# Performance work log

Measured on AMD Instinct MI355X. Metric: run time of the kernel, lower is better.

The kernel has to match this reference:

```python
import jax, jax.numpy as jnp
import numpy as np

B, S, D_MODEL = 4, 2048, 1024
NUM_HEADS, HEAD_DIM = 16, 64
EPS = 1e-6


def setup_inputs() -> dict:
    key = jax.random.key(0)
    ks = jax.random.split(key, 6)
    hd = NUM_HEADS * HEAD_DIM
    scale_in = 1.0 / np.sqrt(D_MODEL)
    scale_hd = 1.0 / np.sqrt(hd)
    return {
        "x": jax.random.normal(ks[0], (B, S, D_MODEL), dtype=jnp.float32),
        "w_q": jax.random.normal(ks[1], (D_MODEL, hd), dtype=jnp.float32) * scale_in,
        "w_k": jax.random.normal(ks[2], (D_MODEL, hd), dtype=jnp.float32) * scale_in,
        "w_v": jax.random.normal(ks[3], (D_MODEL, hd), dtype=jnp.float32) * scale_in,
        "w_proj": jax.random.normal(ks[4], (hd, D_MODEL), dtype=jnp.float32) * scale_hd,
        "b_proj": jax.random.normal(ks[5], (D_MODEL,), dtype=jnp.float32) * 0.01,
        "ln_gamma": jnp.ones((D_MODEL,), dtype=jnp.float32),
        "ln_beta": jnp.zeros((D_MODEL,), dtype=jnp.float32),
    }


def reference(x, w_q, w_k, w_v, w_proj, b_proj, ln_gamma, ln_beta):
    # x: [B, S, D]; project and split heads -> [B, H, S, Dh]
    def split_heads(t):
        b, s, _ = t.shape
        return t.reshape(b, s, NUM_HEADS, HEAD_DIM).transpose(0, 2, 1, 3)

    q = split_heads(x @ w_q)
    k = split_heads(x @ w_k)
    v = split_heads(x @ w_v)

    scale = HEAD_DIM ** (-0.5)
    attn = jnp.einsum("bnqd,bnkd->bnqk", q, k) * scale  # [B, H, S, S]
    attn = jax.nn.softmax(attn, axis=-1)
    o = jnp.einsum("bnqk,bnkd->bnqd", attn, v)  # [B, H, S, Dh]
    o = o.transpose(0, 2, 1, 3).reshape(x.shape[0], x.shape[1], NUM_HEADS * HEAD_DIM)

    # proj + residual (dropout = identity in eval) then LayerNorm(eps=1e-6)
    y = o @ w_proj + b_proj + x
    mean = jnp.mean(y, axis=-1, keepdims=True)
    var = jnp.var(y, axis=-1, keepdims=True)
    y = (y - mean) * jax.lax.rsqrt(var + EPS) * ln_gamma + ln_beta
    return y
```

## Files before the change

kernel.cpp:

```cpp
#include <hip/hip_runtime.h>
#include <hip/hip_fp16.h>


typedef unsigned short u16;
typedef __attribute__((ext_vector_type(8))) u16 u16x8;
typedef __attribute__((ext_vector_type(4))) u16 u16x4;
typedef __attribute__((ext_vector_type(2))) unsigned int u32x2;
typedef __attribute__((ext_vector_type(8))) __bf16 bf16x8;
typedef __attribute__((ext_vector_type(8))) _Float16 f16x8;
typedef __attribute__((ext_vector_type(4))) _Float16 f16x4;
typedef __attribute__((ext_vector_type(2))) _Float16 f16x2;
typedef __attribute__((ext_vector_type(2))) __fp16 hf16x2;
typedef __attribute__((ext_vector_type(4))) float f32x4;

#define SM_C1 0.1803368801111204f

static __device__ __forceinline__ u16 f2bf(float f) {
  union { float f; unsigned int u; } v; v.f = f;
  unsigned int u = v.u;
  return (u16)((u + 0x7fffu + ((u >> 16) & 1u)) >> 16);
}
static __device__ __forceinline__ float bf2f(u16 b) {
  union { unsigned int u; float f; } v; v.u = ((unsigned int)b) << 16;
  return v.f;
}
static __device__ __forceinline__ u16 f2h(float f) {
  union { _Float16 h; u16 u; } v; v.h = (_Float16)f;
  return v.u;
}

static __device__ __forceinline__ void gld16(const u16* g, u16* l) {
  __builtin_amdgcn_global_load_lds((const __attribute__((address_space(1))) void*)g,
                                   (__attribute__((address_space(3))) void*)l, 16, 0, 0);
}

#define QBAR() do { asm volatile("" ::: "memory"); __builtin_amdgcn_s_barrier(); \
                    asm volatile("" ::: "memory"); } while (0)
#define QDRAIN() asm volatile("s_waitcnt vmcnt(0)" ::: "memory")
#define QWAIT6() asm volatile("s_waitcnt vmcnt(6)" ::: "memory")


__global__ __launch_bounds__(256) void k_convx(const float* __restrict__ x,
                                               u16* __restrict__ xbf) {
  int i = (blockIdx.x * 256 + threadIdx.x) * 8;
  float4 a = *(const float4*)(x + i);
  float4 b = *(const float4*)(x + i + 4);
  u16x8 o;
  o[0] = f2bf(a.x); o[1] = f2bf(a.y); o[2] = f2bf(a.z); o[3] = f2bf(a.w);
  o[4] = f2bf(b.x); o[5] = f2bf(b.y); o[6] = f2bf(b.z); o[7] = f2bf(b.w);
  *(u16x8*)(xbf + i) = o;
}

__global__ __launch_bounds__(256) void k_convwT(const float* __restrict__ w0,
                                                const float* __restrict__ w1,
                                                const float* __restrict__ w2,
                                                const float* __restrict__ w3,
                                                u16* __restrict__ o0, u16* __restrict__ o1,
                                                u16* __restrict__ o2, u16* __restrict__ o3) {
  __shared__ float tile[64][65];
  const float* w = blockIdx.z == 0 ? w0 : blockIdx.z == 1 ? w1 : blockIdx.z == 2 ? w2 : w3;
  u16* o = blockIdx.z == 0 ? o0 : blockIdx.z == 1 ? o1 : blockIdx.z == 2 ? o2 : o3;
  const int k0 = blockIdx.x * 64, n0 = blockIdx.y * 64;
  const int t = threadIdx.x;
#pragma unroll
  for (int i = 0; i < 16; i++) {
    int idx = t + 256 * i;
    int k = idx >> 6, n = idx & 63;
    tile[k][n] = w[(k0 + k) * 1024 + n0 + n];
  }
  __syncthreads();
#pragma unroll
  for (int i = 0; i < 16; i++) {
    int idx = t + 256 * i;
    int n = idx >> 6, k = idx & 63;
    o[(n0 + n) * 1024 + k0 + k] = f2bf(tile[k][n]);
  }
}


__global__ __launch_bounds__(512, 2) void k_gemm_qkv(const u16* __restrict__ xbf,
                                                     const u16* __restrict__ wT,
                                                     u16* __restrict__ Qb, u16* __restrict__ Kb,
                                                     u16* __restrict__ VbT) {
  __shared__ alignas(16) u16 As[2][256 * 64];
  __shared__ alignas(16) u16 Bs[2][128 * 64];
  const int t = threadIdx.x;
  const int wv = t >> 6, lane = t & 63, quad = lane >> 4, l16 = lane & 15;
  const int wm = wv >> 1, wn = wv & 1;
  const int m0 = blockIdx.x * 256;
  const int nt = blockIdx.y;
  const int srow = t >> 3;
  const int kg = (t & 7) ^ (srow & 7);
  const u16* aG = xbf + (size_t)(m0 + srow) * 1024 + kg * 8;
  const u16* bG = wT + (size_t)(nt * 128 + srow) * 1024 + kg * 8;
  const int sw = l16 & 7;
  const int ldsDst = wv * 512;

  f32x4 acc[4][4] = {};

  auto STAGE = [&](int tl) {
    const int p_ = tl & 1;
    const int k0_ = tl * 64;
#pragma unroll
    for (int i = 0; i < 4; i++)
      gld16(aG + (size_t)i * 64 * 1024 + k0_, &As[p_][i * 4096 + ldsDst]);
#pragma unroll
    for (int i = 0; i < 2; i++)
      gld16(bG + (size_t)i * 64 * 1024 + k0_, &Bs[p_][i * 4096 + ldsDst]);
  };

  STAGE(0);

#pragma unroll 2
  for (int tile = 0; tile < 16; ++tile) {
    const int p = tile & 1;
    if (tile < 15) { STAGE(tile + 1); QWAIT6(); }
    else           { QDRAIN(); }
    QBAR();

    bf16x8 a[4][2], b[4][2];
#pragma unroll
    for (int f = 0; f < 4; f++)
#pragma unroll
      for (int kk = 0; kk < 2; kk++)
        a[f][kk] = *(const bf16x8*)&As[p][(wm * 64 + f * 16 + l16) * 64 +
                                          ((kk * 4 + quad) ^ sw) * 8];
#pragma unroll
    for (int g = 0; g < 4; g++)
#pragma unroll
      for (int kk = 0; kk < 2; kk++)
        b[g][kk] = *(const bf16x8*)&Bs[p][(wn * 64 + g * 16 + l16) * 64 +
                                          ((kk * 4 + quad) ^ sw) * 8];
#pragma unroll
    for (int f = 0; f < 4; f++)
#pragma unroll
      for (int g = 0; g < 4; g++)
#pragma unroll
        for (int kk = 0; kk < 2; kk++)
          acc[f][g] = __builtin_amdgcn_mfma_f32_16x16x32_bf16(a[f][kk], b[g][kk], acc[f][g], 0, 0, 0);

    QBAR();
  }

  const int sel = nt >> 3;
  const int n0 = (nt & 7) * 128 + wn * 64;
  const int mBase = m0 + wm * 64 + quad * 4;
  if (sel < 2) {
    u16* Ob = sel == 0 ? Qb : Kb;
    const float scl = sel == 0 ? SM_C1 : 1.0f;
#pragma unroll
    for (int f = 0; f < 4; f++)
#pragma unroll
      for (int g = 0; g < 4; g++)
#pragma unroll
        for (int r = 0; r < 4; r++) {
          int m = mBase + f * 16 + r;
          int n = n0 + g * 16 + l16;
          Ob[(size_t)m * 1024 + n] = f2bf(acc[f][g][r] * scl);
        }
  } else {
#pragma unroll
    for (int f = 0; f < 4; f++) {
      int m = mBase + f * 16;
      int bb = m >> 11, s = m & 2047;
#pragma unroll
      for (int g = 0; g < 4; g++) {
        int n = n0 + g * 16 + l16;
        int hh = n >> 6, dh = n & 63;
        u16x4 o;
#pragma unroll
        for (int r = 0; r < 4; r++) o[r] = f2h(acc[f][g][r]);
        *(u16x4*)&VbT[(size_t)(((bb << 4) + hh) * 64 + dh) * 2048 + s] = o;
      }
    }
  }
}


__global__ __launch_bounds__(256) void k_gemm_proj(const u16* __restrict__ Abf,
                                                   const u16* __restrict__ wT,
                                                   const float* __restrict__ x,
                                                   const float* __restrict__ bias,
                                                   u16* __restrict__ ypre) {
  __shared__ alignas(16) u16 Als[128 * 64];
  __shared__ alignas(16) u16 Bls[128 * 64];
  const int t = threadIdx.x;
  const int wv = t >> 6, lane = t & 63, quad = lane >> 4, l16 = lane & 15;
  const int wm = wv >> 1, wn = wv & 1;
  const int m0 = blockIdx.x * 128;
  const int n0t = blockIdx.y * 128;
  const int row = t >> 3;
  const int kg = (t & 7) ^ (row & 7);
  const u16* aG = Abf + (size_t)(m0 + row) * 1024 + kg * 8;
  const u16* bG = wT + (size_t)(n0t + row) * 1024 + kg * 8;
  const int sw = l16 & 7;
  const int aA0 = (wm * 64 + l16) * 64 + ((quad) ^ sw) * 8;
  const int aA1 = (wm * 64 + l16) * 64 + ((4 + quad) ^ sw) * 8;
  const int bA0 = (wn * 64 + l16) * 64 + ((quad) ^ sw) * 8;
  const int bA1 = (wn * 64 + l16) * 64 + ((4 + quad) ^ sw) * 8;

  f32x4 acc[4][4] = {};
  for (int k0 = 0; k0 < 1024; k0 += 64) {
    __syncthreads();
#pragma unroll
    for (int i = 0; i < 4; i++) {
      gld16(aG + i * 32 * 1024 + k0, &Als[(i * 256 + wv * 64) * 8]);
      gld16(bG + i * 32 * 1024 + k0, &Bls[(i * 256 + wv * 64) * 8]);
    }
    __syncthreads();
#pragma unroll
    for (int c = 0; c < 2; c++) {
      bf16x8 a[4], b[4];
#pragma unroll
      for (int f = 0; f < 4; f++) a[f] = *(const bf16x8*)&Als[(c ? aA1 : aA0) + f * 1024];
#pragma unroll
      for (int g = 0; g < 4; g++) b[g] = *(const bf16x8*)&Bls[(c ? bA1 : bA0) + g * 1024];
#pragma unroll
      for (int f = 0; f < 4; f++)
#pragma unroll
        for (int g = 0; g < 4; g++)
          acc[f][g] = __builtin_amdgcn_mfma_f32_16x16x32_bf16(a[f], b[g], acc[f][g], 0, 0, 0);
    }
  }

  const int n0 = n0t + wn * 64;
  const int mBase = m0 + wm * 64 + quad * 4;
#pragma unroll
  for (int g = 0; g < 4; g++) {
    int n = n0 + g * 16 + l16;
    float bn = bias[n];
#pragma unroll
    for (int f = 0; f < 4; f++)
#pragma unroll
      for (int r = 0; r < 4; r++) {
        int m = mBase + f * 16 + r;
        ypre[(size_t)m * 1024 + n] = f2bf(acc[f][g][r] + bn + x[(size_t)m * 1024 + n]);
      }
  }
}


__global__ __launch_bounds__(256, 2) void k_attn(const u16* __restrict__ Qb,
                                                 const u16* __restrict__ Kb,
                                                 const u16* __restrict__ VbT,
                                                 u16* __restrict__ Ob) {
  __shared__ alignas(16) u16 smem[4][64 * 72];
  const int b = blockIdx.x >> 4, h = blockIdx.x & 15;
  const int q0 = blockIdx.y * 256;
  const int t = threadIdx.x;
  const int wave = t >> 6, lane = t & 63, quad = lane >> 4, l16 = lane & 15;
  const int sw = l16 & 7;

  bf16x8 aq[4][2];
#pragma unroll
  for (int qf = 0; qf < 4; qf++)
#pragma unroll
    for (int c = 0; c < 2; c++)
      aq[qf][c] = *(const bf16x8*)&Qb[(size_t)(b * 2048 + q0 + wave * 64 + qf * 16 + l16) * 1024 +
                                      h * 64 + c * 32 + quad * 8];

  f32x4 Oacc[4][4] = {};
  float psum[4] = {};

  const u16* kBase = Kb + (size_t)(b * 2048) * 1024 + h * 64;
  const u16* vBase = VbT + (size_t)((b * 16 + h) * 64) * 2048;

  const int sRow0 = t >> 3, sG0 = (t & 7) ^ (sRow0 & 7);
  const int sRow1 = (256 + t) >> 3, sG1 = (t & 7) ^ (sRow1 & 7);

  auto STAGE = [&](int kt, int p) {
    const int kv = kt * 64;
    u16* Kls = smem[p];
    u16* Vls = smem[2 + p];
    gld16(kBase + (size_t)(kv + sRow0) * 1024 + sG0 * 8, &Kls[(wave * 64) * 8]);
    gld16(kBase + (size_t)(kv + sRow1) * 1024 + sG1 * 8, &Kls[(256 + wave * 64) * 8]);
    gld16(vBase + (size_t)sRow0 * 2048 + kv + sG0 * 8, &Vls[(wave * 64) * 8]);
    gld16(vBase + (size_t)sRow1 * 2048 + kv + sG1 * 8, &Vls[(256 + wave * 64) * 8]);
  };

  STAGE(0, 0);
  QDRAIN();
  QBAR();

  for (int kt = 0; kt < 32; kt++) {
    const int p = kt & 1;
    u16* Kls = smem[p];
    u16* Vls = smem[2 + p];
    if (kt < 31) STAGE(kt + 1, p ^ 1);

    f32x4 st[4][4];
#pragma unroll
    for (int qf = 0; qf < 4; qf++)
#pragma unroll
      for (int f = 0; f < 4; f++) st[qf][f] = f32x4{0.f, 0.f, 0.f, 0.f};
#pragma unroll
    for (int c = 0; c < 2; c++) {
      bf16x8 bk[4];
#pragma unroll
      for (int f = 0; f < 4; f++)
        bk[f] = *(const bf16x8*)&Kls[(f * 16 + l16) * 64 + ((c * 4 + quad) ^ sw) * 8];
#pragma unroll
      for (int qf = 0; qf < 4; qf++)
#pragma unroll
        for (int f = 0; f < 4; f++)
          st[qf][f] = __builtin_amdgcn_mfma_f32_16x16x32_bf16(bk[f], aq[qf][c], st[qf][f], 0, 0, 0);
    }

    f16x8 va[2][4];
#pragma unroll
    for (int kf = 0; kf < 2; kf++)
#pragma unroll
      for (int g = 0; g < 4; g++)
        va[kf][g] = *(const f16x8*)&Vls[(g * 16 + l16) * 64 + ((kf * 4 + quad) ^ sw) * 8];

#pragma unroll
    for (int qf = 0; qf < 4; qf++) {
      union PK { hf16x2 r; f16x2 v; __half2 h; unsigned int u; };
      PK e01[4], e23[4];
      __half2 it2 = __half2{__half(0.f), __half(0.f)};
#pragma unroll
      for (int f = 0; f < 4; f++) {
        PK a01, a23;
        a01.r = __builtin_amdgcn_cvt_pkrtz(st[qf][f][0], st[qf][f][1]);
        a23.r = __builtin_amdgcn_cvt_pkrtz(st[qf][f][2], st[qf][f][3]);
        e01[f].h = h2exp2(a01.h);
        e23[f].h = h2exp2(a23.h);
        it2 = __hadd2(it2, __hadd2(e01[f].h, e23[f].h));
      }
      psum[qf] += __low2float(it2) + __high2float(it2);
#pragma unroll
      for (int kf = 0; kf < 2; kf++) {
        u32x2 sa = __builtin_amdgcn_permlane32_swap(e01[2 * kf].u, e01[2 * kf + 1].u, false, false);
        u32x2 sb = __builtin_amdgcn_permlane32_swap(e23[2 * kf].u, e23[2 * kf + 1].u, false, false);
        u32x2 ta = __builtin_amdgcn_permlane16_swap(sa[0], sa[1], false, false);
        u32x2 tb = __builtin_amdgcn_permlane16_swap(sb[0], sb[1], false, false);
        union { unsigned int u[4]; f16x8 v; } pb;
        pb.u[0] = ta[0];
        pb.u[1] = tb[0];
        pb.u[2] = ta[1];
        pb.u[3] = tb[1];
#pragma unroll
        for (int g = 0; g < 4; g++)
          Oacc[qf][g] = __builtin_amdgcn_mfma_f32_16x16x32_f16(va[kf][g], pb.v, Oacc[qf][g], 0, 0, 0);
      }
    }

    QDRAIN();
    QBAR();
  }

  float inv[4];
#pragma unroll
  for (int qf = 0; qf < 4; qf++) {
    float v = psum[qf];
    v += __shfl_xor(v, 16);
    v += __shfl_xor(v, 32);
    inv[qf] = 1.f / v;
  }

  u16* Ols = (u16*)smem;
#pragma unroll
  for (int qf = 0; qf < 4; qf++)
#pragma unroll
    for (int g = 0; g < 4; g++) {
      u16x4 o;
#pragma unroll
      for (int r = 0; r < 4; r++) o[r] = f2bf(Oacc[qf][g][r] * inv[qf]);
      *(u16x4*)&Ols[(wave * 64 + qf * 16 + l16) * 72 + g * 16 + quad * 4] = o;
    }
  __syncthreads();
  u16* gO = Ob + (size_t)(b * 2048 + q0 + t) * 1024 + h * 64;
#pragma unroll
  for (int j = 0; j < 8; j++)
    *(u16x8*)(gO + j * 8) = *(const u16x8*)&Ols[t * 72 + j * 8];
}


__global__ __launch_bounds__(256) void k_ln(const u16* __restrict__ y,
                                            const float* __restrict__ g,
                                            const float* __restrict__ bt,
                                            float* __restrict__ out) {
  const int row = blockIdx.x;
  const int t = threadIdx.x;
  u16x4 rv = *(const u16x4*)(y + row * 1024 + t * 4);
  float vx = bf2f(rv[0]), vy = bf2f(rv[1]), vz = bf2f(rv[2]), vw = bf2f(rv[3]);
  float s1 = vx + vy + vz + vw;
  float s2 = vx * vx + vy * vy + vz * vz + vw * vw;
#pragma unroll
  for (int off = 32; off; off >>= 1) {
    s1 += __shfl_down(s1, off);
    s2 += __shfl_down(s2, off);
  }
  __shared__ float red[10];
  const int wave = t >> 6, lane = t & 63;
  if (lane == 0) { red[wave] = s1; red[4 + wave] = s2; }
  __syncthreads();
  if (t == 0) {
    float a = red[0] + red[1] + red[2] + red[3];
    float bsum = red[4] + red[5] + red[6] + red[7];
    float mean = a * (1.f / 1024.f);
    float var = bsum * (1.f / 1024.f) - mean * mean;
    red[8] = mean;
    red[9] = rsqrtf(var + 1e-6f);
  }
  __syncthreads();
  float mean = red[8], iv = red[9];
  float4 gv = *(const float4*)(g + t * 4);
  float4 bv = *(const float4*)(bt + t * 4);
  float4 o;
  o.x = (vx - mean) * iv * gv.x + bv.x;
  o.y = (vy - mean) * iv * gv.y + bv.y;
  o.z = (vz - mean) * iv * gv.z + bv.z;
  o.w = (vw - mean) * iv * gv.w + bv.w;
  *(float4*)(out + row * 1024 + t * 4) = o;
}


extern "C" void kernel_launch(void* const* d_in, const int* in_sizes, int n_in,
                              void* d_out, int out_size, void* d_ws, size_t ws_size,
                              hipStream_t stream) {
  const float* x  = (const float*)d_in[0];
  const float* wq = (const float*)d_in[1];
  const float* wk = (const float*)d_in[2];
  const float* wv = (const float*)d_in[3];
  const float* wp = (const float*)d_in[4];
  const float* bp = (const float*)d_in[5];
  const float* g  = (const float*)d_in[6];
  const float* bt = (const float*)d_in[7];
  float* out = (float*)d_out;
  char* ws = (char*)d_ws;

  u16* xbf = (u16*)(ws);
  u16* wqT = (u16*)(ws + (16 << 20));
  u16* wkT = wqT + (size_t)1024 * 1024;
  u16* wvT = wqT + (size_t)2048 * 1024;
  u16* wpT = (u16*)(ws + (22 << 20));
  u16* Qb  = (u16*)(ws + (24 << 20));
  u16* Kb  = (u16*)(ws + (40 << 20));
  u16* VbT = (u16*)(ws + (56 << 20));
  u16* Ob  = (u16*)(ws);
  u16* ypre = (u16*)(ws + (24 << 20));

  k_convx<<<4096, 256, 0, stream>>>(x, xbf);
  k_convwT<<<dim3(16, 16, 4), 256, 0, stream>>>(wq, wk, wv, wp, wqT, wkT, wvT, wpT);
  k_gemm_qkv<<<dim3(32, 24), 512, 0, stream>>>(xbf, wqT, Qb, Kb, VbT);
  k_attn<<<dim3(64, 8), 256, 0, stream>>>(Qb, Kb, VbT, Ob);
  k_gemm_proj<<<dim3(64, 8), 256, 0, stream>>>(Ob, wpT, x, bp, ypre);
  k_ln<<<8192, 256, 0, stream>>>(ypre, g, bt, out);
}
```

Baseline: 272.0 us.

## Merge conversion kernels, double-buffer proj GEMM, halve attention query tile

The x and weight conversion kernels are merged into one launch so one kernel launch goes away. The projection GEMM moves to 512 threads with 256x128 tiles and a double-buffered LDS pipeline that overlaps global loads with MFMA work. The attention kernel processes 128 queries per block instead of 256, doubling the grid and allowing 4 blocks per CU for more occupancy. In exchange, K/V tiles are reloaded twice as often across blocks.

After: 279.6 us. 2.8% more time.

```diff
diff --git a/kernel.cpp b/kernel.cpp
--- a/kernel.cpp
+++ b/kernel.cpp
@@ -40,28 +40,31 @@
 #define QWAIT6() asm volatile("s_waitcnt vmcnt(6)" ::: "memory")
 
 
-__global__ __launch_bounds__(256) void k_convx(const float* __restrict__ x,
-                                               u16* __restrict__ xbf) {
-  int i = (blockIdx.x * 256 + threadIdx.x) * 8;
-  float4 a = *(const float4*)(x + i);
-  float4 b = *(const float4*)(x + i + 4);
-  u16x8 o;
-  o[0] = f2bf(a.x); o[1] = f2bf(a.y); o[2] = f2bf(a.z); o[3] = f2bf(a.w);
-  o[4] = f2bf(b.x); o[5] = f2bf(b.y); o[6] = f2bf(b.z); o[7] = f2bf(b.w);
-  *(u16x8*)(xbf + i) = o;
-}
-
-__global__ __launch_bounds__(256) void k_convwT(const float* __restrict__ w0,
-                                                const float* __restrict__ w1,
-                                                const float* __restrict__ w2,
-                                                const float* __restrict__ w3,
-                                                u16* __restrict__ o0, u16* __restrict__ o1,
-                                                u16* __restrict__ o2, u16* __restrict__ o3) {
+__global__ __launch_bounds__(256) void k_conv(const float* __restrict__ x,
+                                              u16* __restrict__ xbf,
+                                              const float* __restrict__ w0,
+                                              const float* __restrict__ w1,
+                                              const float* __restrict__ w2,
+                                              const float* __restrict__ w3,
+                                              u16* __restrict__ o0, u16* __restrict__ o1,
+                                              u16* __restrict__ o2, u16* __restrict__ o3) {
   __shared__ float tile[64][65];
-  const float* w = blockIdx.z == 0 ? w0 : blockIdx.z == 1 ? w1 : blockIdx.z == 2 ? w2 : w3;
-  u16* o = blockIdx.z == 0 ? o0 : blockIdx.z == 1 ? o1 : blockIdx.z == 2 ? o2 : o3;
-  const int k0 = blockIdx.x * 64, n0 = blockIdx.y * 64;
   const int t = threadIdx.x;
+  if (blockIdx.x < 4096) {
+    int i = (blockIdx.x * 256 + t) * 8;
+    float4 a = *(const float4*)(x + i);
+    float4 b = *(const float4*)(x + i + 4);
+    u16x8 o;
+    o[0] = f2bf(a.x); o[1] = f2bf(a.y); o[2] = f2bf(a.z); o[3] = f2bf(a.w);
+    o[4] = f2bf(b.x); o[5] = f2bf(b.y); o[6] = f2bf(b.z); o[7] = f2bf(b.w);
+    *(u16x8*)(xbf + i) = o;
+    return;
+  }
+  const int id = blockIdx.x - 4096;
+  const int z = id >> 8, rem = id & 255;
+  const int k0 = (rem & 15) * 64, n0 = (rem >> 4) * 64;
+  const float* w = z == 0 ? w0 : z == 1 ? w1 : z == 2 ? w2 : w3;
+  u16* o = z == 0 ? o0 : z == 1 ? o1 : z == 2 ? o2 : o3;
 #pragma unroll
   for (int i = 0; i < 16; i++) {
     int idx = t + 256 * i;
@@ -177,50 +180,69 @@
 }
 
 
-__global__ __launch_bounds__(256) void k_gemm_proj(const u16* __restrict__ Abf,
-                                                   const u16* __restrict__ wT,
-                                                   const float* __restrict__ x,
-                                                   const float* __restrict__ bias,
-                                                   u16* __restrict__ ypre) {
-  __shared__ alignas(16) u16 Als[128 * 64];
-  __shared__ alignas(16) u16 Bls[128 * 64];
+__global__ __launch_bounds__(512, 2) void k_gemm_proj(const u16* __restrict__ Abf,
+                                                      const u16* __restrict__ wT,
+                                                      const float* __restrict__ x,
+                                                      const float* __restrict__ bias,
+                                                      u16* __restrict__ ypre) {
+  __shared__ alignas(16) u16 As[2][256 * 64];
+  __shared__ alignas(16) u16 Bs[2][128 * 64];
   const int t = threadIdx.x;
   const int wv = t >> 6, lane = t & 63, quad = lane >> 4, l16 = lane & 15;
   const int wm = wv >> 1, wn = wv & 1;
-  const int m0 = blockIdx.x * 128;
+  const int m0 = blockIdx.x * 256;
   const int n0t = blockIdx.y * 128;
-  const int row = t >> 3;
-  const int kg = (t & 7) ^ (row & 7);
-  const u16* aG = Abf + (size_t)(m0 + row) * 1024 + kg * 8;
-  const u16* bG = wT + (size_t)(n0t + row) * 1024 + kg * 8;
+  const int srow = t >> 3;
+  const int kg = (t & 7) ^ (srow & 7);
+  const u16* aG = Abf + (size_t)(m0 + srow) * 1024 + kg * 8;
+  const u16* bG = wT + (size_t)(n0t + srow) * 1024 + kg * 8;
   const int sw = l16 & 7;
-  const int aA0 = (wm * 64 + l16) * 64 + ((quad) ^ sw) * 8;
-  const int aA1 = (wm * 64 + l16) * 64 + ((4 + quad) ^ sw) * 8;
-  const int bA0 = (wn * 64 + l16) * 64 + ((quad) ^ sw) * 8;
-  const int bA1 = (wn * 64 + l16) * 64 + ((4 + quad) ^ sw) * 8;
+  const int ldsDst = wv * 512;
 
   f32x4 acc[4][4] = {};
-  for (int k0 = 0; k0 < 1024; k0 += 64) {
-    __syncthreads();
-#pragma unroll
-    for (int i = 0; i < 4; i++) {
-      gld16(aG + i * 32 * 1024 + k0, &Als[(i * 256 + wv * 64) * 8]);
-      gld16(bG + i * 32 * 1024 + k0, &Bls[(i * 256 + wv * 64) * 8]);
-    }
-    __syncthreads();
-#pragma unroll
-    for (int c = 0; c < 2; c++) {
-      bf16x8 a[4], b[4];
-#pragma unroll
-      for (int f = 0; f < 4; f++) a[f] = *(const bf16x8*)&Als[(c ? aA1 : aA0) + f * 1024];
-#pragma unroll
-      for (int g = 0; g < 4; g++) b[g] = *(const bf16x8*)&Bls[(c ? bA1 : bA0) + g * 1024];
-#pragma unroll
-      for (int f = 0; f < 4; f++)
-#pragma unroll
-        for (int g = 0; g < 4; g++)
-          acc[f][g] = __builtin_amdgcn_mfma_f32_16x16x32_bf16(a[f], b[g], acc[f][g], 0, 0, 0);
-    }
+
+  auto STAGE = [&](int tl) {
+    const int p_ = tl & 1;
+    const int k0_ = tl * 64;
+#pragma unroll
+    for (int i = 0; i < 4; i++)
+      gld16(aG + (size_t)i * 64 * 1024 + k0_, &As[p_][i * 4096 + ldsDst]);
+#pragma unroll
+    for (int i = 0; i < 2; i++)
+      gld16(bG + (size_t)i * 64 * 1024 + k0_, &Bs[p_][i * 4096 + ldsDst]);
+  };
+
+  STAGE(0);
+
+#pragma unroll 2
+  for (int tile = 0; tile < 16; ++tile) {
+    const int p = tile & 1;
+    if (tile < 15) { STAGE(tile + 1); QWAIT6(); }
+    else           { QDRAIN(); }
+    QBAR();
+
+    bf16x8 a[4][2], b[4][2];
+#pragma unroll
+    for (int f = 0; f < 4; f++)
+#pragma unroll
+      for (int kk = 0; kk < 2; kk++)
+        a[f][kk] = *(const bf16x8*)&As[p][(wm * 64 + f * 16 + l16) * 64 +
+                                          ((kk * 4 + quad) ^ sw) * 8];
+#pragma unroll
+    for (int g = 0; g < 4; g++)
+#pragma unroll
+      for (int kk = 0; kk < 2; kk++)
+        b[g][kk] = *(const bf16x8*)&Bs[p][(wn * 64 + g * 16 + l16) * 64 +
+                                          ((kk * 4 + quad) ^ sw) * 8];
+#pragma unroll
+    for (int f = 0; f < 4; f++)
+#pragma unroll
+      for (int g = 0; g < 4; g++)
+#pragma unroll
+        for (int kk = 0; kk < 2; kk++)
+          acc[f][g] = __builtin_amdgcn_mfma_f32_16x16x32_bf16(a[f][kk], b[g][kk], acc[f][g], 0, 0, 0);
+
+    QBAR();
   }
 
   const int n0 = n0t + wn * 64;
@@ -240,27 +262,27 @@
 }
 
 
-__global__ __launch_bounds__(256, 2) void k_attn(const u16* __restrict__ Qb,
+__global__ __launch_bounds__(256, 4) void k_attn(const u16* __restrict__ Qb,
                                                  const u16* __restrict__ Kb,
                                                  const u16* __restrict__ VbT,
                                                  u16* __restrict__ Ob) {
   __shared__ alignas(16) u16 smem[4][64 * 72];
   const int b = blockIdx.x >> 4, h = blockIdx.x & 15;
-  const int q0 = blockIdx.y * 256;
+  const int q0 = blockIdx.y * 128;
   const int t = threadIdx.x;
   const int wave = t >> 6, lane = t & 63, quad = lane >> 4, l16 = lane & 15;
   const int sw = l16 & 7;
 
-  bf16x8 aq[4][2];
-#pragma unroll
-  for (int qf = 0; qf < 4; qf++)
+  bf16x8 aq[2][2];
+#pragma unroll
+  for (int qf = 0; qf < 2; qf++)
 #pragma unroll
     for (int c = 0; c < 2; c++)
-      aq[qf][c] = *(const bf16x8*)&Qb[(size_t)(b * 2048 + q0 + wave * 64 + qf * 16 + l16) * 1024 +
+      aq[qf][c] = *(const bf16x8*)&Qb[(size_t)(b * 2048 + q0 + wave * 32 + qf * 16 + l16) * 1024 +
                                       h * 64 + c * 32 + quad * 8];
 
-  f32x4 Oacc[4][4] = {};
-  float psum[4] = {};
+  f32x4 Oacc[2][4] = {};
+  float psum[2] = {};
 
   const u16* kBase = Kb + (size_t)(b * 2048) * 1024 + h * 64;
   const u16* vBase = VbT + (size_t)((b * 16 + h) * 64) * 2048;
@@ -288,9 +310,9 @@
     u16* Vls = smem[2 + p];
     if (kt < 31) STAGE(kt + 1, p ^ 1);
 
-    f32x4 st[4][4];
-#pragma unroll
-    for (int qf = 0; qf < 4; qf++)
+    f32x4 st[2][4];
+#pragma unroll
+    for (int qf = 0; qf < 2; qf++)
 #pragma unroll
       for (int f = 0; f < 4; f++) st[qf][f] = f32x4{0.f, 0.f, 0.f, 0.f};
 #pragma unroll
@@ -300,7 +322,7 @@
       for (int f = 0; f < 4; f++)
         bk[f] = *(const bf16x8*)&Kls[(f * 16 + l16) * 64 + ((c * 4 + quad) ^ sw) * 8];
 #pragma unroll
-      for (int qf = 0; qf < 4; qf++)
+      for (int qf = 0; qf < 2; qf++)
 #pragma unroll
         for (int f = 0; f < 4; f++)
           st[qf][f] = __builtin_amdgcn_mfma_f32_16x16x32_bf16(bk[f], aq[qf][c], st[qf][f], 0, 0, 0);
@@ -314,7 +336,7 @@
         va[kf][g] = *(const f16x8*)&Vls[(g * 16 + l16) * 64 + ((kf * 4 + quad) ^ sw) * 8];
 
 #pragma unroll
-    for (int qf = 0; qf < 4; qf++) {
+    for (int qf = 0; qf < 2; qf++) {
       union PK { hf16x2 r; f16x2 v; __half2 h; unsigned int u; };
       PK e01[4], e23[4];
       __half2 it2 = __half2{__half(0.f), __half(0.f)};
@@ -349,9 +371,9 @@
     QBAR();
   }
 
-  float inv[4];
-#pragma unroll
-  for (int qf = 0; qf < 4; qf++) {
+  float inv[2];
+#pragma unroll
+  for (int qf = 0; qf < 2; qf++) {
     float v = psum[qf];
     v += __shfl_xor(v, 16);
     v += __shfl_xor(v, 32);
@@ -360,19 +382,20 @@
 
   u16* Ols = (u16*)smem;
 #pragma unroll
-  for (int qf = 0; qf < 4; qf++)
+  for (int qf = 0; qf < 2; qf++)
 #pragma unroll
     for (int g = 0; g < 4; g++) {
       u16x4 o;
 #pragma unroll
       for (int r = 0; r < 4; r++) o[r] = f2bf(Oacc[qf][g][r] * inv[qf]);
-      *(u16x4*)&Ols[(wave * 64 + qf * 16 + l16) * 72 + g * 16 + quad * 4] = o;
+      *(u16x4*)&Ols[(wave * 32 + qf * 16 + l16) * 72 + g * 16 + quad * 4] = o;
     }
   __syncthreads();
-  u16* gO = Ob + (size_t)(b * 2048 + q0 + t) * 1024 + h * 64;
-#pragma unroll
-  for (int j = 0; j < 8; j++)
-    *(u16x8*)(gO + j * 8) = *(const u16x8*)&Ols[t * 72 + j * 8];
+  const int orow = t >> 1, ocol = (t & 1) * 32;
+  u16* gO = Ob + (size_t)(b * 2048 + q0 + orow) * 1024 + h * 64 + ocol;
+#pragma unroll
+  for (int j = 0; j < 4; j++)
+    *(u16x8*)(gO + j * 8) = *(const u16x8*)&Ols[orow * 72 + ocol + j * 8];
 }
 
 
@@ -441,10 +464,9 @@
   u16* Ob  = (u16*)(ws);
   u16* ypre = (u16*)(ws + (24 << 20));
 
-  k_convx<<<4096, 256, 0, stream>>>(x, xbf);
-  k_convwT<<<dim3(16, 16, 4), 256, 0, stream>>>(wq, wk, wv, wp, wqT, wkT, wvT, wpT);
+  k_conv<<<5120, 256, 0, stream>>>(x, xbf, wq, wk, wv, wp, wqT, wkT, wvT, wpT);
   k_gemm_qkv<<<dim3(32, 24), 512, 0, stream>>>(xbf, wqT, Qb, Kb, VbT);
-  k_attn<<<dim3(64, 8), 256, 0, stream>>>(Qb, Kb, VbT, Ob);
-  k_gemm_proj<<<dim3(64, 8), 256, 0, stream>>>(Ob, wpT, x, bp, ypre);
+  k_attn<<<dim3(64, 16), 256, 0, stream>>>(Qb, Kb, VbT, Ob);
+  k_gemm_proj<<<dim3(32, 8), 512, 0, stream>>>(Ob, wpT, x, bp, ypre);
   k_ln<<<8192, 256, 0, stream>>>(ypre, g, bt, out);
 }
```
